# Kernel tuning notes

Hardware: AMD Instinct MI355X
Metric: run time of the kernel (lower is better)

The kernel has to match this reference:

```python
import jax, jax.numpy as jnp
import numpy as np

DIM = 1024
NUM_HEADS = 16
HEAD_DIM = DIM // NUM_HEADS  # 64
SCALE = float(np.sqrt(HEAD_DIM))


def setup_inputs() -> dict:
    key = jax.random.key(0)
    k1, k2, k3, k4 = jax.random.split(key, 4)
    B, N = 2, 2048
    x = jax.random.normal(k1, (B, N, DIM), dtype=jnp.float32)
    # torch nn.Linear weights are [out_features, in_features]
    w_qkv = jax.random.normal(k2, (3 * DIM, DIM), dtype=jnp.float32) * (1.0 / np.sqrt(DIM))
    w_proj = jax.random.normal(k3, (DIM, DIM), dtype=jnp.float32) * (1.0 / np.sqrt(DIM))
    b_proj = jax.random.normal(k4, (DIM,), dtype=jnp.float32) * 0.02
    return {"x": x, "w_qkv": w_qkv, "w_proj": w_proj, "b_proj": b_proj}


def reference(x, w_qkv, w_proj, b_proj):
    B, N, C = x.shape
    H, D = NUM_HEADS, HEAD_DIM
    # qkv linear (no bias): [B,N,3C]
    qkv = jnp.einsum('bnc,oc->bno', x, w_qkv)
    qkv = qkv.reshape(B, N, 3, H, D).transpose(2, 0, 3, 1, 4)  # [3,B,H,N,D]
    q, k, v = qkv[0], qkv[1], qkv[2]
    attn = jnp.einsum('bhnd,bhmd->bhnm', q, k) / SCALE  # [B,H,N,N]
    attn = jax.nn.softmax(attn, axis=-1)
    out = jnp.einsum('bhnm,bhmd->bhnd', attn, v)  # [B,H,N,D]
    out = out.transpose(0, 2, 1, 3).reshape(B, N, C)
    return jnp.einsum('bnc,oc->bno', out, w_proj) + b_proj
```

## Files before the change

### kernel.cpp

```cpp
#include <hip/hip_runtime.h>


typedef __bf16 bf16x8 __attribute__((ext_vector_type(8)));
typedef __bf16 bf16x4 __attribute__((ext_vector_type(4)));
typedef float f32x4 __attribute__((ext_vector_type(4)));
typedef unsigned int u32;
typedef u32 u32x4 __attribute__((ext_vector_type(4)));

#define NTOK 2048
#define MFMA16(a, b, c) __builtin_amdgcn_mfma_f32_16x16x32_bf16((a), (b), (c), 0, 0, 0)

#define WAITBAR(N)                                         \
    asm volatile("s_waitcnt vmcnt(" #N ")" ::: "memory"); \
    __builtin_amdgcn_s_barrier();                          \
    __builtin_amdgcn_sched_barrier(0)

__device__ __forceinline__ unsigned short f2bf(float f) {
    unsigned int u = __float_as_uint(f);
    u = (u + 0x7FFFu + ((u >> 16) & 1u)) >> 16;
    return (unsigned short)u;
}

__device__ __forceinline__ u32 cvt_pk(float lo, float hi) {
    u32 r;
    asm("v_cvt_pk_bf16_f32 %0, %1, %2" : "=v"(r) : "v"(lo), "v"(hi));
    return r;
}

__device__ __forceinline__ float hw_exp2(float x) {
#if __has_builtin(__builtin_amdgcn_exp2f)
    return __builtin_amdgcn_exp2f(x);
#else
    float r;
    asm("v_exp_f32 %0, %1" : "=v"(r) : "v"(x));
    return r;
#endif
}

__device__ __forceinline__ void gload16(const void* g, void* l) {
    __builtin_amdgcn_global_load_lds(
        (__attribute__((address_space(1))) void*)(g),
        (__attribute__((address_space(3))) void*)(l), 16, 0, 0);
}

__global__ __launch_bounds__(256) void cast3_kernel(
    const float* __restrict__ x, const float* __restrict__ wq,
    const float* __restrict__ wp, unsigned short* __restrict__ xb,
    unsigned short* __restrict__ wqb, unsigned short* __restrict__ wpb) {
    const int NX = 1048576, NWQ = 786432;
    int i = blockIdx.x * 256 + threadIdx.x;
    const float* src;
    unsigned short* dst;
    int j;
    if (i < NX) { src = x; dst = xb; j = i; }
    else if (i < NX + NWQ) { src = wq; dst = wqb; j = i - NX; }
    else { src = wp; dst = wpb; j = i - NX - NWQ; }
    const float4 v = reinterpret_cast<const float4*>(src)[j];
    ushort4 o;
    o.x = f2bf(v.x); o.y = f2bf(v.y); o.z = f2bf(v.z); o.w = f2bf(v.w);
    reinterpret_cast<ushort4*>(dst)[j] = o;
}

template <int EPI>
__global__ __launch_bounds__(512) void gemm_bt_kernel(
    const unsigned short* __restrict__ A, const unsigned short* __restrict__ B,
    int K, int Ncols,
    unsigned short* __restrict__ q_out, unsigned short* __restrict__ k_out,
    unsigned short* __restrict__ vt_out,
    float* __restrict__ c_out, const float* __restrict__ bias) {
    __shared__ __align__(16) char smem[49152];
    const int tid = threadIdx.x;
    const int l = tid & 63;
    const int wid = tid >> 6;
    const int c = l & 15, g = l >> 4;
    const int wr = wid >> 2, wc = wid & 3;
    const int m0 = blockIdx.x * 128, n0 = blockIdx.y * 128;

    f32x4 acc[4][2] = {};

    const int srow = tid >> 2;
    const int sc16 = (tid & 3) ^ (srow & 3);
    auto STAGE = [&](int bi, int kt) {
        gload16(A + (size_t)(m0 + srow) * K + kt + sc16 * 8,
                smem + bi * 8192 + wid * 1024);
        gload16(B + (size_t)(n0 + srow) * K + kt + sc16 * 8,
                smem + 24576 + bi * 8192 + wid * 1024);
    };

    auto COMPUTE = [&](int bi) {
        const char* bA = smem + bi * 8192;
        const char* bB = smem + 24576 + bi * 8192;
        bf16x8 af[4], bfr[2];
#pragma unroll
        for (int m = 0; m < 4; ++m) {
            const int row = wr * 64 + m * 16 + c;
            af[m] = *(const bf16x8*)(bA + row * 64 + (g ^ (row & 3)) * 16);
        }
#pragma unroll
        for (int n = 0; n < 2; ++n) {
            const int row = wc * 32 + n * 16 + c;
            bfr[n] = *(const bf16x8*)(bB + row * 64 + (g ^ (row & 3)) * 16);
        }
#pragma unroll
        for (int m = 0; m < 4; ++m)
#pragma unroll
            for (int n = 0; n < 2; ++n)
                acc[m][n] = MFMA16(af[m], bfr[n], acc[m][n]);
    };

    const int NK = K >> 5;
    STAGE(0, 0);
    STAGE(1, 32);
    int cb = 0, sb = 2;
    for (int it = 0; it < NK - 2; ++it) {
        WAITBAR(2);
        STAGE(sb, (it + 2) * 32);
        COMPUTE(cb);
        cb = cb == 2 ? 0 : cb + 1;
        sb = sb == 2 ? 0 : sb + 1;
    }
    WAITBAR(2);
    COMPUTE(cb);
    cb = cb == 2 ? 0 : cb + 1;
    WAITBAR(0);
    COMPUTE(cb);

    if (EPI == 0 && n0 >= 2048) {
        __syncthreads();
#pragma unroll
        for (int m = 0; m < 4; ++m) {
            const int tl0 = wr * 64 + m * 16 + g * 4;
#pragma unroll
            for (int n = 0; n < 2; ++n) {
                const int oc = wc * 32 + n * 16 + c;
                bf16x4 pv;
#pragma unroll
                for (int r = 0; r < 4; ++r) pv[r] = (__bf16)acc[m][n][r];
                *(bf16x4*)(smem + oc * 256 + ((tl0 * 2) ^ ((oc & 7) << 4))) = pv;
            }
        }
        __syncthreads();
        const int b = m0 >> 11;
        const int mloc = m0 & 2047;
#pragma unroll
        for (int qq = 0; qq < 4; ++qq) {
            const int ci = qq * 512 + tid;
            const int oc = ci >> 4, j16 = ci & 15;
            const int o = n0 + oc;
            const int head = b * 16 + ((o >> 6) & 15), d = o & 63;
            const bf16x4* src = (const bf16x4*)(smem + oc * 256 +
                                                ((j16 * 16) ^ ((oc & 7) << 4)));
            const int tl8 = j16 * 8;
            const int tpb = (tl8 & ~63) | (tl8 & 0x20) | ((tl8 & 0x10) >> 2) |
                            ((tl8 & 0x08) << 1);
            unsigned short* orow = vt_out + ((size_t)head * 64 + d) * NTOK + mloc;
            *(bf16x4*)(orow + tpb) = src[0];
            *(bf16x4*)(orow + tpb + 8) = src[1];
        }
        return;
    }

#pragma unroll
    for (int m = 0; m < 4; ++m) {
        const int gmb = m0 + wr * 64 + m * 16 + (g << 2);
#pragma unroll
        for (int n = 0; n < 2; ++n) {
            const int gn = n0 + wc * 32 + n * 16 + c;
            if (EPI == 0) {
                const int which = gn >> 10;
                const int h = (gn >> 6) & 15, d = gn & 63;
#pragma unroll
                for (int r = 0; r < 4; ++r) {
                    const int gm = gmb + r;
                    const int head = ((gm >> 11) << 4) | h;
                    const int t = gm & 2047;
                    const float v = acc[m][n][r];
                    if (which == 0)
                        q_out[((size_t)head * NTOK + t) * 64 + d] =
                            f2bf(v * 0.18033688011f);
                    else
                        k_out[((size_t)head * NTOK + t) * 64 + d] = f2bf(v);
                }
            } else {
                const float bv = bias[gn];
#pragma unroll
                for (int r = 0; r < 4; ++r)
                    c_out[(size_t)(gmb + r) * Ncols + gn] = acc[m][n][r] + bv;
            }
        }
    }
}

__global__ __launch_bounds__(256) void attn_kernel(
    const unsigned short* __restrict__ Qb, const unsigned short* __restrict__ Kb,
    const unsigned short* __restrict__ Vt, unsigned short* __restrict__ Ob) {
    __shared__ __align__(16) unsigned short ldsK[2][64 * 64];
    __shared__ __align__(16) unsigned short ldsV[2][64 * 64];

    const int tid = threadIdx.x, l = tid & 63, wid = tid >> 6;
    const int c = l & 15, g = l >> 4;
    const int head = blockIdx.x;
    const int q0 = blockIdx.y * 128 + wid * 32;

    const unsigned short* Qh = Qb + (size_t)head * NTOK * 64;
    const unsigned short* Kh = Kb + (size_t)head * NTOK * 64;
    const unsigned short* Vh = Vt + (size_t)head * 64 * NTOK;

    bf16x8 qf[2][2];
#pragma unroll
    for (int mq = 0; mq < 2; ++mq)
#pragma unroll
        for (int kk = 0; kk < 2; ++kk)
            qf[mq][kk] = *(const bf16x8*)(Qh + (size_t)(q0 + mq * 16 + c) * 64 +
                                          kk * 32 + g * 8);

    f32x4 o_acc[2][4] = {};
    f32x4 lsum[2] = {};

    const int srow = tid >> 3;

    auto STAGE = [&](int buf, int kbase) {
#pragma unroll
        for (int r = 0; r < 2; ++r) {
            const int row = r * 32 + srow;
            const int slot = (tid & 7) ^ (row & 7);
            gload16(Kh + (size_t)(kbase + row) * 64 + slot * 8,
                    (char*)ldsK[buf] + wid * 1024 + r * 4096);
            gload16(Vh + (size_t)row * NTOK + kbase + slot * 8,
                    (char*)ldsV[buf] + wid * 1024 + r * 4096);
        }
    };

    STAGE(0, 0);
    __syncthreads();

    int cur = 0;
    for (int it = 0; it < 32; ++it) {
        if (it + 1 < 32) STAGE(cur ^ 1, (it + 1) * 64);

        f32x4 s0[4] = {}, s1[4] = {};
#pragma unroll
        for (int mk = 0; mk < 4; ++mk) {
            const int row = mk * 16 + c;
#pragma unroll
            for (int kk = 0; kk < 2; ++kk) {
                const int slot = (kk * 4 + g) ^ (row & 7);
                const bf16x8 kf =
                    *(const bf16x8*)((const char*)ldsK[cur] + row * 128 + slot * 16);
                s0[mk] = MFMA16(kf, qf[0][kk], s0[mk]);
                s1[mk] = MFMA16(kf, qf[1][kk], s1[mk]);
            }
        }

        u32x4 pw0[2], pw1[2];
#pragma unroll
        for (int mk = 0; mk < 4; ++mk) {
            const int kv = mk >> 1, dw = (mk & 1) * 2;
            {
                f32x4 e;
                e[0] = hw_exp2(s0[mk][0]); e[1] = hw_exp2(s0[mk][1]);
                e[2] = hw_exp2(s0[mk][2]); e[3] = hw_exp2(s0[mk][3]);
                lsum[0] += e;
                pw0[kv][dw + 0] = cvt_pk(e[0], e[1]);
                pw0[kv][dw + 1] = cvt_pk(e[2], e[3]);
            }
            {
                f32x4 e;
                e[0] = hw_exp2(s1[mk][0]); e[1] = hw_exp2(s1[mk][1]);
                e[2] = hw_exp2(s1[mk][2]); e[3] = hw_exp2(s1[mk][3]);
                lsum[1] += e;
                pw1[kv][dw + 0] = cvt_pk(e[0], e[1]);
                pw1[kv][dw + 1] = cvt_pk(e[2], e[3]);
            }
        }

#pragma unroll
        for (int dm = 0; dm < 4; ++dm) {
            const int row = dm * 16 + c;
#pragma unroll
            for (int kv = 0; kv < 2; ++kv) {
                const int slot = (kv * 4 + g) ^ (row & 7);
                const bf16x8 vt =
                    *(const bf16x8*)((const char*)ldsV[cur] + row * 128 + slot * 16);
                o_acc[0][dm] = MFMA16(vt, __builtin_bit_cast(bf16x8, pw0[kv]),
                                      o_acc[0][dm]);
                o_acc[1][dm] = MFMA16(vt, __builtin_bit_cast(bf16x8, pw1[kv]),
                                      o_acc[1][dm]);
            }
        }
        __syncthreads();
        cur ^= 1;
    }

    const int b = head >> 4, h = head & 15;
#pragma unroll
    for (int mq = 0; mq < 2; ++mq) {
        float lr = (lsum[mq][0] + lsum[mq][1]) + (lsum[mq][2] + lsum[mq][3]);
        lr += __shfl_xor(lr, 16);
        lr += __shfl_xor(lr, 32);
        const float inv = 1.f / lr;
        unsigned short* orow =
            Ob + ((size_t)b * NTOK + q0 + mq * 16 + c) * 1024 + h * 64;
#pragma unroll
        for (int dm = 0; dm < 4; ++dm) {
            bf16x4 ov;
#pragma unroll
            for (int r = 0; r < 4; ++r) ov[r] = (__bf16)(o_acc[mq][dm][r] * inv);
            *(bf16x4*)(orow + dm * 16 + g * 4) = ov;
        }
    }
}

extern "C" void kernel_launch(void* const* d_in, const int* in_sizes, int n_in,
                              void* d_out, int out_size, void* d_ws, size_t ws_size,
                              hipStream_t stream) {
    const float* x = (const float*)d_in[0];
    const float* w_qkv = (const float*)d_in[1];
    const float* w_proj = (const float*)d_in[2];
    const float* b_proj = (const float*)d_in[3];
    float* out = (float*)d_out;

    char* ws = (char*)d_ws;
    const size_t MB = 1 << 20;
    unsigned short* xb = (unsigned short*)(ws);
    unsigned short* wqkvb = (unsigned short*)(ws + 8 * MB);
    unsigned short* wpb = (unsigned short*)(ws + 14 * MB);
    unsigned short* Qb = (unsigned short*)(ws + 16 * MB);
    unsigned short* Kb = (unsigned short*)(ws + 24 * MB);
    unsigned short* Vt = (unsigned short*)(ws + 32 * MB);
    unsigned short* attnb = xb;

    cast3_kernel<<<8192, 256, 0, stream>>>(x, w_qkv, w_proj, xb, wqkvb, wpb);

    gemm_bt_kernel<0><<<dim3(32, 24), 512, 0, stream>>>(
        xb, wqkvb, 1024, 3072, Qb, Kb, Vt, nullptr, nullptr);

    attn_kernel<<<dim3(32, 16), 256, 0, stream>>>(Qb, Kb, Vt, attnb);

    gemm_bt_kernel<1><<<dim3(32, 8), 512, 0, stream>>>(
        attnb, wpb, 1024, 1024, nullptr, nullptr, nullptr, out, b_proj);
}
```

Baseline: 108.1 us.

## Triple-buffer K/V tiles and software-pipeline QK^T one iteration ahead

Moves from two LDS buffers to three and prefetches two tiles ahead. The QK^T MFMAs for the next tile are interleaved with the exp/PV work of the current tile, using ping-pong score registers. The per-iteration __syncthreads is replaced by a vmcnt wait plus barrier. The aim is to overlap the softmax VALU work with matrix ops and to hide global-load latency, at the cost of more LDS and more live registers.

```diff
diff --git a/kernel.cpp b/kernel.cpp
--- a/kernel.cpp
+++ b/kernel.cpp
@@ -194,8 +194,8 @@
 __global__ __launch_bounds__(256) void attn_kernel(
     const unsigned short* __restrict__ Qb, const unsigned short* __restrict__ Kb,
     const unsigned short* __restrict__ Vt, unsigned short* __restrict__ Ob) {
-    __shared__ __align__(16) unsigned short ldsK[2][64 * 64];
-    __shared__ __align__(16) unsigned short ldsV[2][64 * 64];
+    __shared__ __align__(16) unsigned short ldsK[3][64 * 64];
+    __shared__ __align__(16) unsigned short ldsV[3][64 * 64];
 
     const int tid = threadIdx.x, l = tid & 63, wid = tid >> 6;
     const int c = l & 15, g = l >> 4;
@@ -219,77 +219,86 @@
 
     const int srow = tid >> 3;
 
-    auto STAGE = [&](int buf, int kbase) {
+    auto STAGE = [&](int bi, int kbase) {
 #pragma unroll
         for (int r = 0; r < 2; ++r) {
             const int row = r * 32 + srow;
             const int slot = (tid & 7) ^ (row & 7);
             gload16(Kh + (size_t)(kbase + row) * 64 + slot * 8,
-                    (char*)ldsK[buf] + wid * 1024 + r * 4096);
+                    (char*)ldsK + bi * 8192 + wid * 1024 + r * 4096);
             gload16(Vh + (size_t)row * NTOK + kbase + slot * 8,
-                    (char*)ldsV[buf] + wid * 1024 + r * 4096);
-        }
+                    (char*)ldsV + bi * 8192 + wid * 1024 + r * 4096);
+        }
+    };
+
+    auto QKBLK = [&](const char* bK, int mk, f32x4& a0, f32x4& a1) {
+        const int row = mk * 16 + c;
+        f32x4 t0 = {}, t1 = {};
+#pragma unroll
+        for (int kk = 0; kk < 2; ++kk) {
+            const int slot = (kk * 4 + g) ^ (c & 7);
+            const bf16x8 kf = *(const bf16x8*)(bK + row * 128 + slot * 16);
+            t0 = MFMA16(kf, qf[0][kk], t0);
+            t1 = MFMA16(kf, qf[1][kk], t1);
+        }
+        a0 = t0; a1 = t1;
     };
 
     STAGE(0, 0);
-    __syncthreads();
-
-    int cur = 0;
-    for (int it = 0; it < 32; ++it) {
-        if (it + 1 < 32) STAGE(cur ^ 1, (it + 1) * 64);
-
-        f32x4 s0[4] = {}, s1[4] = {};
+    STAGE(1, 64);
+    WAITBAR(4);
+
+    f32x4 sA[2][4], sB[2][4];
+#pragma unroll
+    for (int mk = 0; mk < 4; ++mk)
+        QKBLK((const char*)ldsK, mk, sA[0][mk], sA[1][mk]);
+
+    auto STEP = [&](int t, f32x4 (&sc)[2][4], f32x4 (&sn)[2][4]) {
+        WAITBAR(0);
+        if (t + 2 < 32) STAGE((t + 2) % 3, (t + 2) * 64);
+        const char* bK = (const char*)ldsK + ((t + 1) % 3) * 8192;
+        const char* bV = (const char*)ldsV + (t % 3) * 8192;
+        const bool doQK = (t + 1 < 32);
+        u32x4 pw0[2], pw1[2];
 #pragma unroll
         for (int mk = 0; mk < 4; ++mk) {
-            const int row = mk * 16 + c;
-#pragma unroll
-            for (int kk = 0; kk < 2; ++kk) {
-                const int slot = (kk * 4 + g) ^ (row & 7);
-                const bf16x8 kf =
-                    *(const bf16x8*)((const char*)ldsK[cur] + row * 128 + slot * 16);
-                s0[mk] = MFMA16(kf, qf[0][kk], s0[mk]);
-                s1[mk] = MFMA16(kf, qf[1][kk], s1[mk]);
-            }
-        }
-
-        u32x4 pw0[2], pw1[2];
-#pragma unroll
-        for (int mk = 0; mk < 4; ++mk) {
+            if (doQK) QKBLK(bK, mk, sn[0][mk], sn[1][mk]);
             const int kv = mk >> 1, dw = (mk & 1) * 2;
             {
                 f32x4 e;
-                e[0] = hw_exp2(s0[mk][0]); e[1] = hw_exp2(s0[mk][1]);
-                e[2] = hw_exp2(s0[mk][2]); e[3] = hw_exp2(s0[mk][3]);
+                e[0] = hw_exp2(sc[0][mk][0]); e[1] = hw_exp2(sc[0][mk][1]);
+                e[2] = hw_exp2(sc[0][mk][2]); e[3] = hw_exp2(sc[0][mk][3]);
                 lsum[0] += e;
                 pw0[kv][dw + 0] = cvt_pk(e[0], e[1]);
                 pw0[kv][dw + 1] = cvt_pk(e[2], e[3]);
             }
             {
                 f32x4 e;
-                e[0] = hw_exp2(s1[mk][0]); e[1] = hw_exp2(s1[mk][1]);
-                e[2] = hw_exp2(s1[mk][2]); e[3] = hw_exp2(s1[mk][3]);
+                e[0] = hw_exp2(sc[1][mk][0]); e[1] = hw_exp2(sc[1][mk][1]);
+                e[2] = hw_exp2(sc[1][mk][2]); e[3] = hw_exp2(sc[1][mk][3]);
                 lsum[1] += e;
                 pw1[kv][dw + 0] = cvt_pk(e[0], e[1]);
                 pw1[kv][dw + 1] = cvt_pk(e[2], e[3]);
             }
         }
-
 #pragma unroll
         for (int dm = 0; dm < 4; ++dm) {
             const int row = dm * 16 + c;
 #pragma unroll
             for (int kv = 0; kv < 2; ++kv) {
-                const int slot = (kv * 4 + g) ^ (row & 7);
-                const bf16x8 vt =
-                    *(const bf16x8*)((const char*)ldsV[cur] + row * 128 + slot * 16);
+                const int slot = (kv * 4 + g) ^ (c & 7);
+                const bf16x8 vt = *(const bf16x8*)(bV + row * 128 + slot * 16);
                 o_acc[0][dm] = MFMA16(vt, __builtin_bit_cast(bf16x8, pw0[kv]),
                                       o_acc[0][dm]);
                 o_acc[1][dm] = MFMA16(vt, __builtin_bit_cast(bf16x8, pw1[kv]),
                                       o_acc[1][dm]);
             }
         }
-        __syncthreads();
-        cur ^= 1;
+    };
+
+    for (int t = 0; t < 32; t += 2) {
+        STEP(t, sA, sB);
+        STEP(t + 1, sB, sA);
     }
 
     const int b = head >> 4, h = head & 15;
```

Measured after the change: 106.7 us, median of 2. No clear change (-1.3%).

## Double per-wave query rows in attention and remap GEMM workgroups across XCDs

Applied to the files above, without the earlier changes.

The attention kernel now gives each wave 64 query rows instead of 32 and halves the grid. Each K and V fragment read from LDS is therefore reused across four query tiles, which cuts LDS traffic and K/V staging per output. The GEMM kernels remap the workgroup index so that consecutive blocks are spread across the 8 XCDs, aiming for better L2 locality. In exchange, the attention kernel needs more registers (larger accumulators and score arrays) and launches fewer blocks (256), which may reduce occupancy on 256 CUs.

```diff
diff --git a/kernel.cpp b/kernel.cpp
--- a/kernel.cpp
+++ b/kernel.cpp
@@ -74,7 +74,11 @@
     const int wid = tid >> 6;
     const int c = l & 15, g = l >> 4;
     const int wr = wid >> 2, wc = wid & 3;
-    const int m0 = blockIdx.x * 128, n0 = blockIdx.y * 128;
+
+    const int nwg = gridDim.x * gridDim.y;
+    int wg = blockIdx.y * gridDim.x + blockIdx.x;
+    wg = (wg & 7) * (nwg >> 3) + (wg >> 3);
+    const int m0 = (wg % gridDim.x) * 128, n0 = (wg / gridDim.x) * 128;
 
     f32x4 acc[4][2] = {};
 
@@ -200,22 +204,22 @@
     const int tid = threadIdx.x, l = tid & 63, wid = tid >> 6;
     const int c = l & 15, g = l >> 4;
     const int head = blockIdx.x;
-    const int q0 = blockIdx.y * 128 + wid * 32;
+    const int q0 = blockIdx.y * 256 + wid * 64;
 
     const unsigned short* Qh = Qb + (size_t)head * NTOK * 64;
     const unsigned short* Kh = Kb + (size_t)head * NTOK * 64;
     const unsigned short* Vh = Vt + (size_t)head * 64 * NTOK;
 
-    bf16x8 qf[2][2];
-#pragma unroll
-    for (int mq = 0; mq < 2; ++mq)
+    bf16x8 qf[4][2];
+#pragma unroll
+    for (int mq = 0; mq < 4; ++mq)
 #pragma unroll
         for (int kk = 0; kk < 2; ++kk)
             qf[mq][kk] = *(const bf16x8*)(Qh + (size_t)(q0 + mq * 16 + c) * 64 +
                                           kk * 32 + g * 8);
 
-    f32x4 o_acc[2][4] = {};
-    f32x4 lsum[2] = {};
+    f32x4 o_acc[4][4] = {};
+    f32x4 lsum[4] = {};
 
     const int srow = tid >> 3;
 
@@ -234,58 +238,53 @@
     STAGE(0, 0);
     __syncthreads();
 
+    const f32x4 fz = {};
     int cur = 0;
     for (int it = 0; it < 32; ++it) {
         if (it + 1 < 32) STAGE(cur ^ 1, (it + 1) * 64);
 
-        f32x4 s0[4] = {}, s1[4] = {};
+        f32x4 s[4][4];
 #pragma unroll
         for (int mk = 0; mk < 4; ++mk) {
             const int row = mk * 16 + c;
-#pragma unroll
-            for (int kk = 0; kk < 2; ++kk) {
-                const int slot = (kk * 4 + g) ^ (row & 7);
-                const bf16x8 kf =
-                    *(const bf16x8*)((const char*)ldsK[cur] + row * 128 + slot * 16);
-                s0[mk] = MFMA16(kf, qf[0][kk], s0[mk]);
-                s1[mk] = MFMA16(kf, qf[1][kk], s1[mk]);
-            }
-        }
-
-        u32x4 pw0[2], pw1[2];
-#pragma unroll
-        for (int mk = 0; mk < 4; ++mk) {
-            const int kv = mk >> 1, dw = (mk & 1) * 2;
-            {
+            const bf16x8 kf0 =
+                *(const bf16x8*)((const char*)ldsK[cur] + row * 128 + ((0 + g) ^ (c & 7)) * 16);
+            const bf16x8 kf1 =
+                *(const bf16x8*)((const char*)ldsK[cur] + row * 128 + ((4 + g) ^ (c & 7)) * 16);
+#pragma unroll
+            for (int mq = 0; mq < 4; ++mq) {
+                const f32x4 t = MFMA16(kf0, qf[mq][0], fz);
+                s[mq][mk] = MFMA16(kf1, qf[mq][1], t);
+            }
+        }
+
+        u32x4 pw[4][2];
+#pragma unroll
+        for (int mq = 0; mq < 4; ++mq)
+#pragma unroll
+            for (int mk = 0; mk < 4; ++mk) {
                 f32x4 e;
-                e[0] = hw_exp2(s0[mk][0]); e[1] = hw_exp2(s0[mk][1]);
-                e[2] = hw_exp2(s0[mk][2]); e[3] = hw_exp2(s0[mk][3]);
-                lsum[0] += e;
-                pw0[kv][dw + 0] = cvt_pk(e[0], e[1]);
-                pw0[kv][dw + 1] = cvt_pk(e[2], e[3]);
-            }
-            {
-                f32x4 e;
-                e[0] = hw_exp2(s1[mk][0]); e[1] = hw_exp2(s1[mk][1]);
-                e[2] = hw_exp2(s1[mk][2]); e[3] = hw_exp2(s1[mk][3]);
-                lsum[1] += e;
-                pw1[kv][dw + 0] = cvt_pk(e[0], e[1]);
-                pw1[kv][dw + 1] = cvt_pk(e[2], e[3]);
-            }
-        }
+                e[0] = hw_exp2(s[mq][mk][0]); e[1] = hw_exp2(s[mq][mk][1]);
+                e[2] = hw_exp2(s[mq][mk][2]); e[3] = hw_exp2(s[mq][mk][3]);
+                lsum[mq] += e;
+                const int kv = mk >> 1, dw = (mk & 1) * 2;
+                pw[mq][kv][dw + 0] = cvt_pk(e[0], e[1]);
+                pw[mq][kv][dw + 1] = cvt_pk(e[2], e[3]);
+            }
 
 #pragma unroll
         for (int dm = 0; dm < 4; ++dm) {
             const int row = dm * 16 + c;
-#pragma unroll
-            for (int kv = 0; kv < 2; ++kv) {
-                const int slot = (kv * 4 + g) ^ (row & 7);
-                const bf16x8 vt =
-                    *(const bf16x8*)((const char*)ldsV[cur] + row * 128 + slot * 16);
-                o_acc[0][dm] = MFMA16(vt, __builtin_bit_cast(bf16x8, pw0[kv]),
-                                      o_acc[0][dm]);
-                o_acc[1][dm] = MFMA16(vt, __builtin_bit_cast(bf16x8, pw1[kv]),
-                                      o_acc[1][dm]);
+            const bf16x8 vt0 =
+                *(const bf16x8*)((const char*)ldsV[cur] + row * 128 + ((0 + g) ^ (c & 7)) * 16);
+            const bf16x8 vt1 =
+                *(const bf16x8*)((const char*)ldsV[cur] + row * 128 + ((4 + g) ^ (c & 7)) * 16);
+#pragma unroll
+            for (int mq = 0; mq < 4; ++mq) {
+                o_acc[mq][dm] = MFMA16(vt0, __builtin_bit_cast(bf16x8, pw[mq][0]),
+                                       o_acc[mq][dm]);
+                o_acc[mq][dm] = MFMA16(vt1, __builtin_bit_cast(bf16x8, pw[mq][1]),
+                                       o_acc[mq][dm]);
             }
         }
         __syncthreads();
@@ -294,7 +293,7 @@
 
     const int b = head >> 4, h = head & 15;
 #pragma unroll
-    for (int mq = 0; mq < 2; ++mq) {
+    for (int mq = 0; mq < 4; ++mq) {
         float lr = (lsum[mq][0] + lsum[mq][1]) + (lsum[mq][2] + lsum[mq][3]);
         lr += __shfl_xor(lr, 16);
         lr += __shfl_xor(lr, 32);
@@ -335,7 +334,7 @@
     gemm_bt_kernel<0><<<dim3(32, 24), 512, 0, stream>>>(
         xb, wqkvb, 1024, 3072, Qb, Kb, Vt, nullptr, nullptr);
 
-    attn_kernel<<<dim3(32, 16), 256, 0, stream>>>(Qb, Kb, Vt, attnb);
+    attn_kernel<<<dim3(32, 8), 256, 0, stream>>>(Qb, Kb, Vt, attnb);
 
     gemm_bt_kernel<1><<<dim3(32, 8), 512, 0, stream>>>(
         attnb, wpb, 1024, 1024, nullptr, nullptr, nullptr, out, b_proj);
```

Result: slower. 120.1 us (+11.1%).
